# Kernel optimization log

Hardware: AMD Instinct MI355X
Metric: run time of the kernel (lower is better)

Reference implementation:

```python
import jax, jax.numpy as jnp
import numpy as np

B, C, H, W, D = 16, 512, 14, 14, 8000  # batch, channels(=input_dim1=input_dim2), spatial, output_dim


def _sketch_matrix(seed_h, seed_s, input_dim, output_dim):
    # Reproduce the module's count-sketch matrix generation (np.random.seed based).
    np.random.seed(seed_h)
    rand_h = np.random.randint(output_dim, size=input_dim)
    np.random.seed(seed_s)
    rand_s = (2 * np.random.randint(2, size=input_dim) - 1).astype(np.float32)
    M = np.zeros((input_dim, output_dim), dtype=np.float32)
    M[np.arange(input_dim), rand_h] = rand_s  # one-hot-per-row with sign
    return jnp.asarray(M)


def setup_inputs() -> dict:
    key = jax.random.key(0)
    x = jax.random.normal(key, (B, C, H, W), dtype=jnp.float32)
    S1 = _sketch_matrix(1, 3, C, D)
    S2 = _sketch_matrix(5, 7, C, D)
    return {"x": x, "S1": S1, "S2": S2}


def reference(x, S1, S2):
    b, c, h, w = x.shape
    # NCHW -> (B*H*W, C)
    flat = jnp.transpose(x, (0, 2, 3, 1)).reshape(-1, c)
    sketch1 = flat @ S1  # [BHW, D]
    sketch2 = flat @ S2  # [BHW, D]
    # circular convolution of the two count-sketches via FFT
    f1 = jnp.fft.fft(sketch1, axis=-1)
    f2 = jnp.fft.fft(sketch2, axis=-1)
    cbp_flat = jnp.fft.ifft(f1 * f2, axis=-1).real.astype(x.dtype)
    cbp = cbp_flat.reshape(b, h, w, -1)
    # sum_pool=True: reduce over spatial dims -> [B, D]
    return cbp.sum(axis=(1, 2))
```

## Files before the change

### kernel.cpp

```cpp
#include <hip/hip_runtime.h>

#define B_DIM 16
#define C_DIM 512
#define HW_DIM 196
#define D_DIM 8000

#define KT 28
#define IT 128
#define JT 64
#define PAD 4

__global__ __launch_bounds__(256) void extract_both(
    const float* __restrict__ S1, const float* __restrict__ S2,
    int* __restrict__ h, float* __restrict__ s) {
    const int row   = blockIdx.x & (C_DIM - 1);
    const int which = blockIdx.x >> 9;
    const float* S  = which ? S2 : S1;
    const float4* rowp = (const float4*)(S + (size_t)row * D_DIM);
    int*   hp = h + which * C_DIM;
    float* sp = s + which * C_DIM;
    for (int j4 = threadIdx.x; j4 < D_DIM / 4; j4 += 256) {
        float4 v = rowp[j4];
        if (v.x != 0.0f) { hp[row] = 4 * j4 + 0; sp[row] = v.x; }
        if (v.y != 0.0f) { hp[row] = 4 * j4 + 1; sp[row] = v.y; }
        if (v.z != 0.0f) { hp[row] = 4 * j4 + 2; sp[row] = v.z; }
        if (v.w != 0.0f) { hp[row] = 4 * j4 + 3; sp[row] = v.w; }
    }
}

__global__ __launch_bounds__(256, 2) void gram_hist(
    const float* __restrict__ x,
    const int* __restrict__ h1, const float* __restrict__ s1,
    const int* __restrict__ h2, const float* __restrict__ s2,
    float* __restrict__ out) {
    const int b  = blockIdx.z;
    const int i0 = blockIdx.y * IT;
    const int j0 = blockIdx.x * JT;
    const float* A = x + (size_t)b * C_DIM * HW_DIM;

    __shared__ float hist[D_DIM];
    __shared__ float At[KT][IT + PAD];
    __shared__ float Bt[KT][JT + PAD];

    const int tid = threadIdx.x;
    const int tx  = tid & 15;
    const int ty  = tid >> 4;

    for (int d = tid; d < D_DIM; d += 256) hist[d] = 0.0f;

    float acc[8][4] = {};

    for (int k0 = 0; k0 < HW_DIM; k0 += KT) {
        #pragma unroll
        for (int l = 0; l < 14; ++l) {
            int idx = l * 256 + tid;
            int r   = idx / KT;
            int kk  = idx - r * KT;
            At[kk][r] = A[(size_t)(i0 + r) * HW_DIM + k0 + kk];
        }
        #pragma unroll
        for (int l = 0; l < 7; ++l) {
            int idx = l * 256 + tid;
            int r   = idx / KT;
            int kk  = idx - r * KT;
            Bt[kk][r] = A[(size_t)(j0 + r) * HW_DIM + k0 + kk];
        }
        __syncthreads();

        #pragma unroll
        for (int kk = 0; kk < KT; ++kk) {
            float4 a0 = *(const float4*)&At[kk][ty * 8];
            float4 a1 = *(const float4*)&At[kk][ty * 8 + 4];
            float4 b0 = *(const float4*)&Bt[kk][tx * 4];
            float a[8]  = {a0.x, a0.y, a0.z, a0.w, a1.x, a1.y, a1.z, a1.w};
            float bb[4] = {b0.x, b0.y, b0.z, b0.w};
            #pragma unroll
            for (int u = 0; u < 8; ++u)
                #pragma unroll
                for (int v = 0; v < 4; ++v)
                    acc[u][v] += a[u] * bb[v];
        }
        __syncthreads();
    }

    int hr[8]; float sr[8]; int hc[4]; float sc[4];
    #pragma unroll
    for (int u = 0; u < 8; ++u) {
        hr[u] = h1[i0 + ty * 8 + u];
        sr[u] = s1[i0 + ty * 8 + u];
    }
    #pragma unroll
    for (int v = 0; v < 4; ++v) {
        hc[v] = h2[j0 + tx * 4 + v];
        sc[v] = s2[j0 + tx * 4 + v];
    }
    #pragma unroll
    for (int u = 0; u < 8; ++u)
        #pragma unroll
        for (int v = 0; v < 4; ++v) {
            int bin = hr[u] + hc[v];
            if (bin >= D_DIM) bin -= D_DIM;
            atomicAdd(&hist[bin], sr[u] * sc[v] * acc[u][v]);
        }
    __syncthreads();

    float* outb = out + (size_t)b * D_DIM;
    for (int d = tid; d < D_DIM; d += 256) {
        float v = hist[d];
        if (v != 0.0f) atomicAdd(outb + d, v);
    }
}

extern "C" void kernel_launch(void* const* d_in, const int* in_sizes, int n_in,
                              void* d_out, int out_size, void* d_ws, size_t ws_size,
                              hipStream_t stream) {
    const float* x  = (const float*)d_in[0];
    const float* S1 = (const float*)d_in[1];
    const float* S2 = (const float*)d_in[2];
    float* out = (float*)d_out;

    int*   h = (int*)d_ws;
    float* s = (float*)(h + 2 * C_DIM);

    hipMemsetAsync(d_out, 0, (size_t)out_size * sizeof(float), stream);

    extract_both<<<2 * C_DIM, 256, 0, stream>>>(S1, S2, h, s);

    dim3 grid(C_DIM / JT, C_DIM / IT, B_DIM);
    gram_hist<<<grid, 256, 0, stream>>>(x, h, s, h + C_DIM, s + C_DIM, out);
}
```

Baseline: 138.2 us.

## Use bf16 MFMA for the Gram matrix with padded bf16 prepass

A prep kernel now converts x to bf16 with round-to-nearest-even, padded from 196 to 224 along K, and it also zeroes the output and extracts the sketch hash and sign, replacing the memset and the separate extraction launch. The Gram tile is computed with 16x16x32 bf16 MFMA instructions. Operands are loaded straight from global memory into registers with one step of register prefetch, instead of an fp32 FMA loop staged through shared memory. This cuts FMA issue cost and a launch, but it lowers precision of the Gram products to bf16 inputs and adds an extra pass that writes a bf16 copy of x.

```diff
diff --git a/kernel.cpp b/kernel.cpp
--- a/kernel.cpp
+++ b/kernel.cpp
@@ -4,104 +4,137 @@
 #define C_DIM 512
 #define HW_DIM 196
 #define D_DIM 8000
+#define KP 224
+#define NROW (B_DIM * C_DIM)
 
-#define KT 28
-#define IT 128
-#define JT 64
-#define PAD 4
+typedef __attribute__((ext_vector_type(8))) short short8;
+typedef __attribute__((ext_vector_type(4))) float float4v;
 
-__global__ __launch_bounds__(256) void extract_both(
-    const float* __restrict__ S1, const float* __restrict__ S2,
-    int* __restrict__ h, float* __restrict__ s) {
-    const int row   = blockIdx.x & (C_DIM - 1);
-    const int which = blockIdx.x >> 9;
-    const float* S  = which ? S2 : S1;
-    const float4* rowp = (const float4*)(S + (size_t)row * D_DIM);
-    int*   hp = h + which * C_DIM;
-    float* sp = s + which * C_DIM;
-    for (int j4 = threadIdx.x; j4 < D_DIM / 4; j4 += 256) {
-        float4 v = rowp[j4];
-        if (v.x != 0.0f) { hp[row] = 4 * j4 + 0; sp[row] = v.x; }
-        if (v.y != 0.0f) { hp[row] = 4 * j4 + 1; sp[row] = v.y; }
-        if (v.z != 0.0f) { hp[row] = 4 * j4 + 2; sp[row] = v.z; }
-        if (v.w != 0.0f) { hp[row] = 4 * j4 + 3; sp[row] = v.w; }
+__global__ __launch_bounds__(256) void prep(
+    const float* __restrict__ x, const float* __restrict__ S1,
+    const float* __restrict__ S2,
+    int* __restrict__ h, float* __restrict__ s,
+    unsigned short* __restrict__ xp, float* __restrict__ out) {
+    const int bid = blockIdx.x;
+    const int tid = threadIdx.x;
+    if (bid < 2 * C_DIM) {
+        const int row   = bid & (C_DIM - 1);
+        const int which = bid >> 9;
+        const float4* rowp = (const float4*)((which ? S2 : S1) + (size_t)row * D_DIM);
+        int*   hp = h + which * C_DIM;
+        float* sp = s + which * C_DIM;
+        for (int j4 = tid; j4 < D_DIM / 4; j4 += 256) {
+            float4 v = rowp[j4];
+            if (v.x != 0.0f) { hp[row] = 4 * j4 + 0; sp[row] = v.x; }
+            if (v.y != 0.0f) { hp[row] = 4 * j4 + 1; sp[row] = v.y; }
+            if (v.z != 0.0f) { hp[row] = 4 * j4 + 2; sp[row] = v.z; }
+            if (v.w != 0.0f) { hp[row] = 4 * j4 + 3; sp[row] = v.w; }
+        }
+    } else {
+        const int j = bid - 2 * C_DIM;
+        #pragma unroll
+        for (int l = 0; l < 14; ++l) {
+            int idx = l * 256 + tid;
+            int r   = idx / KP;
+            int kk  = idx - r * KP;
+            int row = j * 16 + r;
+            float v = (kk < HW_DIM) ? x[(size_t)row * HW_DIM + kk] : 0.0f;
+            unsigned int u = __float_as_uint(v);
+            u = (u + 0x7FFFu + ((u >> 16) & 1u)) >> 16;
+            xp[(size_t)row * KP + kk] = (unsigned short)u;
+        }
+        if (j < 500) out[j * 256 + tid] = 0.0f;
     }
 }
 
-__global__ __launch_bounds__(256, 2) void gram_hist(
-    const float* __restrict__ x,
+__global__ __launch_bounds__(256) void gram_hist(
+    const unsigned short* __restrict__ xp,
     const int* __restrict__ h1, const float* __restrict__ s1,
     const int* __restrict__ h2, const float* __restrict__ s2,
     float* __restrict__ out) {
     const int b  = blockIdx.z;
-    const int i0 = blockIdx.y * IT;
-    const int j0 = blockIdx.x * JT;
-    const float* A = x + (size_t)b * C_DIM * HW_DIM;
+    const int i0 = blockIdx.y * 128;
+    const int j0 = blockIdx.x * 64;
 
     __shared__ float hist[D_DIM];
-    __shared__ float At[KT][IT + PAD];
-    __shared__ float Bt[KT][JT + PAD];
+    const int tid = threadIdx.x;
+    for (int d = tid; d < D_DIM; d += 256) hist[d] = 0.0f;
+    __syncthreads();
 
-    const int tid = threadIdx.x;
-    const int tx  = tid & 15;
-    const int ty  = tid >> 4;
+    const int w  = tid >> 6;
+    const int l  = tid & 63;
+    const int rA = l & 15;
+    const int g  = l >> 4;
 
-    for (int d = tid; d < D_DIM; d += 256) hist[d] = 0.0f;
+    const unsigned short* base = xp + (size_t)b * C_DIM * KP;
+    const unsigned short* pA[2];
+    const unsigned short* pB[4];
+    #pragma unroll
+    for (int mt = 0; mt < 2; ++mt)
+        pA[mt] = base + (size_t)(i0 + w * 32 + mt * 16 + rA) * KP + g * 8;
+    #pragma unroll
+    for (int nt = 0; nt < 4; ++nt)
+        pB[nt] = base + (size_t)(j0 + nt * 16 + rA) * KP + g * 8;
 
-    float acc[8][4] = {};
+    float4v acc[2][4];
+    #pragma unroll
+    for (int mt = 0; mt < 2; ++mt)
+        #pragma unroll
+        for (int nt = 0; nt < 4; ++nt)
+            acc[mt][nt] = (float4v){0.0f, 0.0f, 0.0f, 0.0f};
 
-    for (int k0 = 0; k0 < HW_DIM; k0 += KT) {
-        #pragma unroll
-        for (int l = 0; l < 14; ++l) {
-            int idx = l * 256 + tid;
-            int r   = idx / KT;
-            int kk  = idx - r * KT;
-            At[kk][r] = A[(size_t)(i0 + r) * HW_DIM + k0 + kk];
+    short8 fa[2], fb[4];
+    #pragma unroll
+    for (int mt = 0; mt < 2; ++mt) fa[mt] = *(const short8*)pA[mt];
+    #pragma unroll
+    for (int nt = 0; nt < 4; ++nt) fb[nt] = *(const short8*)pB[nt];
+
+    #pragma unroll
+    for (int step = 1; step <= 7; ++step) {
+        short8 na[2], nb[4];
+        if (step < 7) {
+            #pragma unroll
+            for (int mt = 0; mt < 2; ++mt) na[mt] = *(const short8*)(pA[mt] + step * 32);
+            #pragma unroll
+            for (int nt = 0; nt < 4; ++nt) nb[nt] = *(const short8*)(pB[nt] + step * 32);
         }
         #pragma unroll
-        for (int l = 0; l < 7; ++l) {
-            int idx = l * 256 + tid;
-            int r   = idx / KT;
-            int kk  = idx - r * KT;
-            Bt[kk][r] = A[(size_t)(j0 + r) * HW_DIM + k0 + kk];
+        for (int mt = 0; mt < 2; ++mt)
+            #pragma unroll
+            for (int nt = 0; nt < 4; ++nt)
+                acc[mt][nt] = __builtin_amdgcn_mfma_f32_16x16x32_bf16(
+                    fa[mt], fb[nt], acc[mt][nt], 0, 0, 0);
+        if (step < 7) {
+            #pragma unroll
+            for (int mt = 0; mt < 2; ++mt) fa[mt] = na[mt];
+            #pragma unroll
+            for (int nt = 0; nt < 4; ++nt) fb[nt] = nb[nt];
         }
-        __syncthreads();
-
-        #pragma unroll
-        for (int kk = 0; kk < KT; ++kk) {
-            float4 a0 = *(const float4*)&At[kk][ty * 8];
-            float4 a1 = *(const float4*)&At[kk][ty * 8 + 4];
-            float4 b0 = *(const float4*)&Bt[kk][tx * 4];
-            float a[8]  = {a0.x, a0.y, a0.z, a0.w, a1.x, a1.y, a1.z, a1.w};
-            float bb[4] = {b0.x, b0.y, b0.z, b0.w};
-            #pragma unroll
-            for (int u = 0; u < 8; ++u)
-                #pragma unroll
-                for (int v = 0; v < 4; ++v)
-                    acc[u][v] += a[u] * bb[v];
-        }
-        __syncthreads();
     }
 
-    int hr[8]; float sr[8]; int hc[4]; float sc[4];
+    int hr[2][4]; float sr[2][4]; int hc[4]; float sc[4];
     #pragma unroll
-    for (int u = 0; u < 8; ++u) {
-        hr[u] = h1[i0 + ty * 8 + u];
-        sr[u] = s1[i0 + ty * 8 + u];
+    for (int mt = 0; mt < 2; ++mt)
+        #pragma unroll
+        for (int r = 0; r < 4; ++r) {
+            int c1 = i0 + w * 32 + mt * 16 + (l >> 4) * 4 + r;
+            hr[mt][r] = h1[c1]; sr[mt][r] = s1[c1];
+        }
+    #pragma unroll
+    for (int nt = 0; nt < 4; ++nt) {
+        int c2 = j0 + nt * 16 + (l & 15);
+        hc[nt] = h2[c2]; sc[nt] = s2[c2];
     }
     #pragma unroll
-    for (int v = 0; v < 4; ++v) {
-        hc[v] = h2[j0 + tx * 4 + v];
-        sc[v] = s2[j0 + tx * 4 + v];
-    }
-    #pragma unroll
-    for (int u = 0; u < 8; ++u)
+    for (int mt = 0; mt < 2; ++mt)
         #pragma unroll
-        for (int v = 0; v < 4; ++v) {
-            int bin = hr[u] + hc[v];
-            if (bin >= D_DIM) bin -= D_DIM;
-            atomicAdd(&hist[bin], sr[u] * sc[v] * acc[u][v]);
-        }
+        for (int nt = 0; nt < 4; ++nt)
+            #pragma unroll
+            for (int r = 0; r < 4; ++r) {
+                int bin = hr[mt][r] + hc[nt];
+                if (bin >= D_DIM) bin -= D_DIM;
+                atomicAdd(&hist[bin], sr[mt][r] * sc[nt] * acc[mt][nt][r]);
+            }
     __syncthreads();
 
     float* outb = out + (size_t)b * D_DIM;
@@ -119,13 +152,12 @@
     const float* S2 = (const float*)d_in[2];
     float* out = (float*)d_out;
 
-    int*   h = (int*)d_ws;
-    float* s = (float*)(h + 2 * C_DIM);
+    int*            h  = (int*)d_ws;
+    float*          s  = (float*)(h + 2 * C_DIM);
+    unsigned short* xp = (unsigned short*)(s + 2 * C_DIM);
 
-    hipMemsetAsync(d_out, 0, (size_t)out_size * sizeof(float), stream);
+    prep<<<2 * C_DIM + NROW / 16, 256, 0, stream>>>(x, S1, S2, h, s, xp, out);
 
-    extract_both<<<2 * C_DIM, 256, 0, stream>>>(S1, S2, h, s);
-
-    dim3 grid(C_DIM / JT, C_DIM / IT, B_DIM);
-    gram_hist<<<grid, 256, 0, stream>>>(x, h, s, h + C_DIM, s + C_DIM, out);
+    dim3 grid(C_DIM / 64, C_DIM / 128, B_DIM);
+    gram_hist<<<grid, 256, 0, stream>>>(xp, h, s, h + C_DIM, s + C_DIM, out);
 }
```

After: 122.4 us. -11.4%, faster.
